# Performance work log

Measured on AMD Instinct MI355X. Metric: run time of the kernel, lower is better.

The kernel has to match this reference:

```python
import jax, jax.numpy as jnp
import numpy as np

MD = 512      # Md = input_dim[0] * ds
L = 31        # spectral bands
SHOTS = 1
HO = jnp.array([0.25, 0.5, 0.25], dtype=jnp.float32)


def spectral_conv3(x, axis):
    # SAME-padded 1x1x3 conv along the spectral axis with symmetric kernel HO.
    # (tf.nn.conv3d and tf.nn.conv3d_transpose coincide for this symmetric kernel.)
    pad = [(0, 0)] * x.ndim
    pad[axis] = (1, 1)
    xp = jnp.pad(x, pad)
    sl = lambda s: tuple(s if a == axis else slice(None) for a in range(x.ndim))
    return HO[0] * xp[sl(slice(0, -2))] + HO[1] * xp[sl(slice(1, -1))] + HO[2] * xp[sl(slice(2, None))]


def setup_inputs() -> dict:
    key = jax.random.key(0)
    k1, k2, k3 = jax.random.split(key, 3)
    X = jax.random.uniform(k1, (1, 1024, 1024, L), dtype=jnp.float32)
    y = jax.random.uniform(k2, (1, MD, MD + L - 1, SHOTS), dtype=jnp.float32)
    H = jax.random.uniform(k3, (1, MD, MD, L, SHOTS), dtype=jnp.float32)
    return {"X": X, "y": y, "H": H}


def reference(X, y, H):
    B = X.shape[0]
    C = MD + L - 1  # detector width after dispersion
    # tf.image.resize (bilinear, half-pixel) -> jax.image.resize bilinear
    Xr = jax.image.resize(X, (B, MD, MD, L), method='bilinear')
    # spectral blur: conv3d with kernel [1,1,3] = HO, SAME padding
    Xc = spectral_conv3(Xr, axis=3)                      # [B,MD,MD,L]
    Xm = H * Xc[..., None]                               # [B,MD,MD,L,S]
    # pad dispersion axis then shear-sum: yn[.,c,s] = sum_i Xm[., c-i, i, s]
    Xp = jnp.pad(Xm, ((0, 0), (0, 0), (0, L - 1), (0, 0), (0, 0)))  # [B,MD,C,L,S]
    cc = jnp.arange(C)
    ii = jnp.arange(L)
    idx = (cc[:, None] - ii[None, :]) % C                # [C,L] roll-with-zero-fill
    yn = Xp[:, :, idx, ii, :].sum(axis=3)                # [B,MD,C,S]
    yn = yn / jnp.max(yn)
    r = yn - y                                           # residual on the detector
    # adjoint shear: Xn[.,c,i,s] = r[., c+i, s]
    idx2 = jnp.arange(MD)[:, None] + ii[None, :]         # [MD,L], max = C-1 (no wrap)
    Xn = r[:, :, idx2, :]                                # [B,MD,MD,L,S]
    # adjoint spectral blur (conv3d_transpose, symmetric kernel == same conv)
    X2 = spectral_conv3(Xn, axis=3)                      # [B,MD,MD,L,S]
    X2 = (H * X2).sum(axis=4)                            # [B,MD,MD,L]
    return X2 / jnp.max(X2)
```

## Files before the change

kernel.cpp:

```cpp
#include <hip/hip_runtime.h>

#define MDIM 512
#define LCH  31
#define CDIM 542
#define INW  1024
#define RS   (INW*LCH)
#define NELEM (MDIM*MDIM*LCH)
#define GB3  2048

#define TNK  32
#define NT   16
#define NPAIR 256

#define PART_OFF 0
#define PART_SZ  (NPAIR*NT*2*128)
#define YN_OFF   (PART_OFF + PART_SZ)
#define PMY_OFF  (YN_OFF + MDIM*CDIM)
#define PMT_OFF  (PMY_OFF + MDIM)
#define SCL_OFF  (PMT_OFF + GB3)

__global__ __launch_bounds__(256) void k1_fused(const float* __restrict__ X,
                                                const float* __restrict__ H,
                                                float* __restrict__ part) {
    __shared__ float xv[2][2048];
    __shared__ float xm[2][32][33];

    const int bid = blockIdx.x;
    const int t   = bid & (NT-1);
    const int p   = bid >> 4;
    const int n0  = t * TNK;
    const int m0  = 2*p;
    const int tid = threadIdx.x;
    const int qa  = 1984*t - 32;

    const float* rp0 = X + (size_t)max(4*p - 1, 0) * RS;
    const float* rp1 = X + (size_t)(4*p    ) * RS;
    const float* rp2 = X + (size_t)(4*p + 1) * RS;
    const float* rp3 = X + (size_t)(4*p + 2) * RS;
    const float* rp4 = X + (size_t)(4*p + 3) * RS;
    const float* rp5 = X + (size_t)min(4*p + 4, INW-1) * RS;

    float wa0=0.125f, wa1=0.375f, wa2=0.375f, wa3=0.125f;
    if (m0 == 0) {
        const float s = 1.0f/0.875f;
        wa0 = 0.f; wa1 = 0.375f*s; wa2 = 0.375f*s; wa3 = 0.125f*s;
    }
    float wb0=0.125f, wb1=0.375f, wb2=0.375f, wb3=0.125f;
    if (m0 + 1 == MDIM-1) {
        const float s = 1.0f/0.875f;
        wb0 = 0.125f*s; wb1 = 0.375f*s; wb2 = 0.375f*s; wb3 = 0.f;
    }

    #pragma unroll
    for (int j = 0; j < 2; ++j) {
        const int u = tid + 256*j;
        int q = qa + 4*u;
        q = min(max(q, 0), RS - 4);
        const float4 r0 = *(const float4*)(rp0 + q);
        const float4 r1 = *(const float4*)(rp1 + q);
        const float4 r2 = *(const float4*)(rp2 + q);
        const float4 r3 = *(const float4*)(rp3 + q);
        const float4 r4 = *(const float4*)(rp4 + q);
        const float4 r5 = *(const float4*)(rp5 + q);
        float4 va, vb;
        va.x = fmaf(wa0,r0.x, fmaf(wa1,r1.x, fmaf(wa2,r2.x, wa3*r3.x)));
        va.y = fmaf(wa0,r0.y, fmaf(wa1,r1.y, fmaf(wa2,r2.y, wa3*r3.y)));
        va.z = fmaf(wa0,r0.z, fmaf(wa1,r1.z, fmaf(wa2,r2.z, wa3*r3.z)));
        va.w = fmaf(wa0,r0.w, fmaf(wa1,r1.w, fmaf(wa2,r2.w, wa3*r3.w)));
        vb.x = fmaf(wb0,r2.x, fmaf(wb1,r3.x, fmaf(wb2,r4.x, wb3*r5.x)));
        vb.y = fmaf(wb0,r2.y, fmaf(wb1,r3.y, fmaf(wb2,r4.y, wb3*r5.y)));
        vb.z = fmaf(wb0,r2.z, fmaf(wb1,r3.z, fmaf(wb2,r4.z, wb3*r5.z)));
        vb.w = fmaf(wb0,r2.w, fmaf(wb1,r3.w, fmaf(wb2,r4.w, wb3*r5.w)));
        *(float4*)&xv[0][4*u] = va;
        *(float4*)&xv[1][4*u] = vb;
    }
    __syncthreads();

    const size_t hbase = ((size_t)m0*MDIM + n0)*LCH;
    for (int idx = tid; idx < 2*TNK*LCH; idx += 256) {
        const int mm = idx >= TNK*LCH;
        const int r2 = mm ? idx - TNK*LCH : idx;
        const int nl = r2 / 31;
        const int l  = r2 - nl*31;
        const int n  = n0 + nl;
        float wx0=0.125f, wx1=0.375f, wx2=0.375f, wx3=0.125f;
        if (n == 0)      wx0 = 0.f;
        if (n == MDIM-1) wx3 = 0.f;
        if (n == 0 || n == MDIM-1) {
            const float s = 1.0f/0.875f;
            wx0*=s; wx1*=s; wx2*=s; wx3*=s;
        }
        const float wb4[4] = {wx0, wx1, wx2, wx3};
        const float* xvm = xv[mm];
        const int ib = 2*nl*31 + l + 1;
        float acc = 0.f;
        #pragma unroll
        for (int b = 0; b < 4; ++b) {
            const float* q = xvm + ib + 31*b;
            float c = 0.5f*q[0];
            if (l > 0)  c += 0.25f*q[-1];
            if (l < 30) c += 0.25f*q[1];
            acc = fmaf(wb4[b], c, acc);
        }
        const float hv = H[hbase + (size_t)mm*(MDIM*LCH) + r2];
        xm[mm][nl][l] = acc * hv;
    }
    __syncthreads();

    if (tid < 248) {
        const int mm = tid >= 124;
        const int r3 = mm ? tid - 124 : tid;
        const int h  = r3 >= 62;
        const int cl = h ? r3 - 62 : r3;
        const int ilo = max(0, cl - (TNK-1));
        const int ihi = min(30, cl);
        const int mid = (ilo + ihi + 1) >> 1;
        const int lo  = h ? mid : ilo;
        const int hi  = h ? ihi : mid - 1;
        float s = 0.f;
        for (int i = lo; i <= hi; ++i)
            s += xm[mm][cl - i][i];
        part[(((size_t)p*NT + t)*2 + mm)*128 + h*64 + cl] = s;
    }
}

__global__ __launch_bounds__(256) void k2_lite(const float* __restrict__ part,
                                               float* __restrict__ yn,
                                               float* __restrict__ pmaxY) {
    const int m = blockIdx.x;
    const int p = m >> 1, mm = m & 1;
    float lmax = -3.4e38f;
    for (int c = threadIdx.x; c < CDIM; c += 256) {
        float s = 0.f;
        const int tlo = max(0, (c - 30) >> 5);
        const int thi = min(NT - 1, c >> 5);
        for (int t = tlo; t <= thi; ++t) {
            const int cl = c - TNK*t;
            const float* pp = part + (((size_t)p*NT + t)*2 + mm)*128;
            s += pp[cl] + pp[64 + cl];
        }
        yn[m*CDIM + c] = s;
        lmax = fmaxf(lmax, s);
    }
    __shared__ float red[256];
    red[threadIdx.x] = lmax; __syncthreads();
    for (int s = 128; s > 0; s >>= 1) {
        if ((int)threadIdx.x < s)
            red[threadIdx.x] = fmaxf(red[threadIdx.x], red[threadIdx.x+s]);
        __syncthreads();
    }
    if (threadIdx.x == 0) pmaxY[m] = red[0];
}

__global__ __launch_bounds__(256) void kmax_reduce(const float* __restrict__ pmax,
                                                   int n,
                                                   float* __restrict__ out_inv) {
    __shared__ float red[256];
    float lmax = -3.4e38f;
    for (int i = threadIdx.x; i < n; i += 256)
        lmax = fmaxf(lmax, pmax[i]);
    red[threadIdx.x] = lmax; __syncthreads();
    for (int s = 128; s > 0; s >>= 1) {
        if ((int)threadIdx.x < s)
            red[threadIdx.x] = fmaxf(red[threadIdx.x], red[threadIdx.x+s]);
        __syncthreads();
    }
    if (threadIdx.x == 0) out_inv[0] = 1.0f / red[0];
}

__device__ __forceinline__ float t_elem(int idx,
                                        const float* __restrict__ yn,
                                        const float* __restrict__ y,
                                        const float* __restrict__ H,
                                        float inv) {
    const int i    = idx % LCH;
    const int rest = idx / LCH;
    const int n    = rest & (MDIM-1);
    const int m    = rest >> 9;
    const int c    = n + i;
    const float* ynr = yn + (size_t)m*CDIM;
    const float* yr  = y  + (size_t)m*CDIM;
    float v = 0.5f * (ynr[c]*inv - yr[c]);
    if (i > 0)     v += 0.25f*(ynr[c-1]*inv - yr[c-1]);
    if (i < LCH-1) v += 0.25f*(ynr[c+1]*inv - yr[c+1]);
    return H[idx]*v;
}

__global__ __launch_bounds__(256) void k3_max(const float* __restrict__ yn,
                                              const float* __restrict__ y,
                                              const float* __restrict__ H,
                                              const float* __restrict__ scl,
                                              float* __restrict__ pmaxT) {
    const float inv = scl[0];
    float lmax = -3.4e38f;
    for (int idx = blockIdx.x*blockDim.x + threadIdx.x; idx < NELEM;
         idx += GB3*256)
        lmax = fmaxf(lmax, t_elem(idx, yn, y, H, inv));
    __shared__ float red[256];
    red[threadIdx.x] = lmax; __syncthreads();
    for (int s = 128; s > 0; s >>= 1) {
        if ((int)threadIdx.x < s)
            red[threadIdx.x] = fmaxf(red[threadIdx.x], red[threadIdx.x+s]);
        __syncthreads();
    }
    if (threadIdx.x == 0) pmaxT[blockIdx.x] = red[0];
}

__global__ __launch_bounds__(256) void k4_out(const float* __restrict__ yn,
                                              const float* __restrict__ y,
                                              const float* __restrict__ H,
                                              const float* __restrict__ scl,
                                              float* __restrict__ out) {
    const float inv  = scl[0];
    const float invT = scl[1];
    for (int idx = blockIdx.x*blockDim.x + threadIdx.x; idx < NELEM;
         idx += GB3*256)
        out[idx] = t_elem(idx, yn, y, H, inv) * invT;
}

extern "C" void kernel_launch(void* const* d_in, const int* in_sizes, int n_in,
                              void* d_out, int out_size, void* d_ws, size_t ws_size,
                              hipStream_t stream) {
    const float* X = (const float*)d_in[0];
    const float* y = (const float*)d_in[1];
    const float* H = (const float*)d_in[2];
    float* out = (float*)d_out;
    float* ws  = (float*)d_ws;

    float* part  = ws + PART_OFF;
    float* yn    = ws + YN_OFF;
    float* pmaxY = ws + PMY_OFF;
    float* pmaxT = ws + PMT_OFF;
    float* scl   = ws + SCL_OFF;

    k1_fused<<<NPAIR*NT, 256, 0, stream>>>(X, H, part);
    k2_lite<<<MDIM, 256, 0, stream>>>(part, yn, pmaxY);
    kmax_reduce<<<1, 256, 0, stream>>>(pmaxY, MDIM, scl);
    k3_max<<<GB3, 256, 0, stream>>>(yn, y, H, scl, pmaxT);
    kmax_reduce<<<1, 256, 0, stream>>>(pmaxT, GB3, scl + 1);
    k4_out<<<GB3, 256, 0, stream>>>(yn, y, H, scl, out);
}
```

Before: 90.79 us.

## Process four output rows per block and fold max reductions into last-block epilogues

```diff
diff --git a/kernel.cpp b/kernel.cpp
--- a/kernel.cpp
+++ b/kernel.cpp
@@ -10,76 +10,76 @@
 
 #define TNK  32
 #define NT   16
-#define NPAIR 256
+#define MGRP 4
+#define NQ   128
 
 #define PART_OFF 0
-#define PART_SZ  (NPAIR*NT*2*128)
+#define PART_SZ  (NQ*NT*MGRP*128)
 #define YN_OFF   (PART_OFF + PART_SZ)
 #define PMY_OFF  (YN_OFF + MDIM*CDIM)
 #define PMT_OFF  (PMY_OFF + MDIM)
 #define SCL_OFF  (PMT_OFF + GB3)
+#define CNT_OFF  (SCL_OFF + 2)
 
 __global__ __launch_bounds__(256) void k1_fused(const float* __restrict__ X,
                                                 const float* __restrict__ H,
-                                                float* __restrict__ part) {
-    __shared__ float xv[2][2048];
-    __shared__ float xm[2][32][33];
+                                                float* __restrict__ part,
+                                                int* __restrict__ cnt) {
+    __shared__ float xv[MGRP][2048];
+    __shared__ float xm[MGRP][32][33];
 
     const int bid = blockIdx.x;
     const int t   = bid & (NT-1);
-    const int p   = bid >> 4;
+    const int g   = bid >> 4;
     const int n0  = t * TNK;
-    const int m0  = 2*p;
     const int tid = threadIdx.x;
     const int qa  = 1984*t - 32;
 
-    const float* rp0 = X + (size_t)max(4*p - 1, 0) * RS;
-    const float* rp1 = X + (size_t)(4*p    ) * RS;
-    const float* rp2 = X + (size_t)(4*p + 1) * RS;
-    const float* rp3 = X + (size_t)(4*p + 2) * RS;
-    const float* rp4 = X + (size_t)(4*p + 3) * RS;
-    const float* rp5 = X + (size_t)min(4*p + 4, INW-1) * RS;
-
-    float wa0=0.125f, wa1=0.375f, wa2=0.375f, wa3=0.125f;
-    if (m0 == 0) {
-        const float s = 1.0f/0.875f;
-        wa0 = 0.f; wa1 = 0.375f*s; wa2 = 0.375f*s; wa3 = 0.125f*s;
-    }
-    float wb0=0.125f, wb1=0.375f, wb2=0.375f, wb3=0.125f;
-    if (m0 + 1 == MDIM-1) {
-        const float s = 1.0f/0.875f;
-        wb0 = 0.125f*s; wb1 = 0.375f*s; wb2 = 0.375f*s; wb3 = 0.f;
-    }
+    if (bid == 0 && tid < 2) cnt[tid] = 0;
+
+    float W[4][4];
+    #pragma unroll
+    for (int k = 0; k < 4; ++k) {
+        W[k][0]=0.125f; W[k][1]=0.375f; W[k][2]=0.375f; W[k][3]=0.125f;
+    }
+    if (g == 0)      { const float s=1.0f/0.875f; W[0][0]=0.f; W[0][1]=0.375f*s; W[0][2]=0.375f*s; W[0][3]=0.125f*s; }
+    if (g == NQ-1)   { const float s=1.0f/0.875f; W[3][3]=0.f; W[3][0]=0.125f*s; W[3][1]=0.375f*s; W[3][2]=0.375f*s; }
+
+    const float* rowp[10];
+    #pragma unroll
+    for (int rr = 0; rr < 10; ++rr)
+        rowp[rr] = X + (size_t)min(max(8*g - 1 + rr, 0), INW-1) * RS;
 
     #pragma unroll
     for (int j = 0; j < 2; ++j) {
         const int u = tid + 256*j;
-        int q = qa + 4*u;
-        q = min(max(q, 0), RS - 4);
-        const float4 r0 = *(const float4*)(rp0 + q);
-        const float4 r1 = *(const float4*)(rp1 + q);
-        const float4 r2 = *(const float4*)(rp2 + q);
-        const float4 r3 = *(const float4*)(rp3 + q);
-        const float4 r4 = *(const float4*)(rp4 + q);
-        const float4 r5 = *(const float4*)(rp5 + q);
-        float4 va, vb;
-        va.x = fmaf(wa0,r0.x, fmaf(wa1,r1.x, fmaf(wa2,r2.x, wa3*r3.x)));
-        va.y = fmaf(wa0,r0.y, fmaf(wa1,r1.y, fmaf(wa2,r2.y, wa3*r3.y)));
-        va.z = fmaf(wa0,r0.z, fmaf(wa1,r1.z, fmaf(wa2,r2.z, wa3*r3.z)));
-        va.w = fmaf(wa0,r0.w, fmaf(wa1,r1.w, fmaf(wa2,r2.w, wa3*r3.w)));
-        vb.x = fmaf(wb0,r2.x, fmaf(wb1,r3.x, fmaf(wb2,r4.x, wb3*r5.x)));
-        vb.y = fmaf(wb0,r2.y, fmaf(wb1,r3.y, fmaf(wb2,r4.y, wb3*r5.y)));
-        vb.z = fmaf(wb0,r2.z, fmaf(wb1,r3.z, fmaf(wb2,r4.z, wb3*r5.z)));
-        vb.w = fmaf(wb0,r2.w, fmaf(wb1,r3.w, fmaf(wb2,r4.w, wb3*r5.w)));
-        *(float4*)&xv[0][4*u] = va;
-        *(float4*)&xv[1][4*u] = vb;
-    }
-    __syncthreads();
-
-    const size_t hbase = ((size_t)m0*MDIM + n0)*LCH;
-    for (int idx = tid; idx < 2*TNK*LCH; idx += 256) {
-        const int mm = idx >= TNK*LCH;
-        const int r2 = mm ? idx - TNK*LCH : idx;
+        const int q = min(max(qa + 4*u, 0), RS - 4);
+        float4 acc[4];
+        #pragma unroll
+        for (int k = 0; k < 4; ++k) acc[k] = make_float4(0.f,0.f,0.f,0.f);
+        #pragma unroll
+        for (int rr = 0; rr < 10; ++rr) {
+            const float4 r = *(const float4*)(rowp[rr] + q);
+            #pragma unroll
+            for (int k = 0; k < 4; ++k) {
+                if (rr >= 2*k && rr <= 2*k + 3) {
+                    const float w = W[k][rr - 2*k];
+                    acc[k].x = fmaf(w, r.x, acc[k].x);
+                    acc[k].y = fmaf(w, r.y, acc[k].y);
+                    acc[k].z = fmaf(w, r.z, acc[k].z);
+                    acc[k].w = fmaf(w, r.w, acc[k].w);
+                }
+            }
+        }
+        #pragma unroll
+        for (int k = 0; k < 4; ++k) *(float4*)&xv[k][4*u] = acc[k];
+    }
+    __syncthreads();
+
+    const size_t hbase = ((size_t)(MGRP*g)*MDIM + n0)*LCH;
+    for (int idx = tid; idx < MGRP*TNK*LCH; idx += 256) {
+        const int mm = idx / (TNK*LCH);
+        const int r2 = idx - mm*(TNK*LCH);
         const int nl = r2 / 31;
         const int l  = r2 - nl*31;
         const int n  = n0 + nl;
@@ -102,33 +102,37 @@
             if (l < 30) c += 0.25f*q[1];
             acc = fmaf(wb4[b], c, acc);
         }
-        const float hv = H[hbase + (size_t)mm*(MDIM*LCH) + r2];
-        xm[mm][nl][l] = acc * hv;
-    }
-    __syncthreads();
-
-    if (tid < 248) {
-        const int mm = tid >= 124;
-        const int r3 = mm ? tid - 124 : tid;
-        const int h  = r3 >= 62;
-        const int cl = h ? r3 - 62 : r3;
-        const int ilo = max(0, cl - (TNK-1));
-        const int ihi = min(30, cl);
-        const int mid = (ilo + ihi + 1) >> 1;
-        const int lo  = h ? mid : ilo;
-        const int hi  = h ? ihi : mid - 1;
-        float s = 0.f;
-        for (int i = lo; i <= hi; ++i)
-            s += xm[mm][cl - i][i];
-        part[(((size_t)p*NT + t)*2 + mm)*128 + h*64 + cl] = s;
+        xm[mm][nl][l] = acc * H[hbase + (size_t)mm*(MDIM*LCH) + r2];
+    }
+    __syncthreads();
+
+    for (int base = 0; base < 496; base += 256) {
+        const int idx = base + tid;
+        if (idx < 496) {
+            const int mm = idx / 124;
+            const int r3 = idx - mm*124;
+            const int h  = r3 >= 62;
+            const int cl = h ? r3 - 62 : r3;
+            const int ilo = max(0, cl - (TNK-1));
+            const int ihi = min(30, cl);
+            const int mid = (ilo + ihi + 1) >> 1;
+            const int lo  = h ? mid : ilo;
+            const int hi  = h ? ihi : mid - 1;
+            float s = 0.f;
+            for (int i = lo; i <= hi; ++i)
+                s += xm[mm][cl - i][i];
+            part[(((size_t)g*NT + t)*MGRP + mm)*128 + h*64 + cl] = s;
+        }
     }
 }
 
 __global__ __launch_bounds__(256) void k2_lite(const float* __restrict__ part,
                                                float* __restrict__ yn,
-                                               float* __restrict__ pmaxY) {
+                                               float* __restrict__ pmaxY,
+                                               float* __restrict__ scl,
+                                               int* __restrict__ cnt) {
     const int m = blockIdx.x;
-    const int p = m >> 1, mm = m & 1;
+    const int g = m >> 2, mm = m & 3;
     float lmax = -3.4e38f;
     for (int c = threadIdx.x; c < CDIM; c += 256) {
         float s = 0.f;
@@ -136,36 +140,39 @@
         const int thi = min(NT - 1, c >> 5);
         for (int t = tlo; t <= thi; ++t) {
             const int cl = c - TNK*t;
-            const float* pp = part + (((size_t)p*NT + t)*2 + mm)*128;
+            const float* pp = part + (((size_t)g*NT + t)*MGRP + mm)*128;
             s += pp[cl] + pp[64 + cl];
         }
         yn[m*CDIM + c] = s;
         lmax = fmaxf(lmax, s);
     }
     __shared__ float red[256];
+    __shared__ int isLast;
     red[threadIdx.x] = lmax; __syncthreads();
     for (int s = 128; s > 0; s >>= 1) {
         if ((int)threadIdx.x < s)
             red[threadIdx.x] = fmaxf(red[threadIdx.x], red[threadIdx.x+s]);
         __syncthreads();
     }
-    if (threadIdx.x == 0) pmaxY[m] = red[0];
-}
-
-__global__ __launch_bounds__(256) void kmax_reduce(const float* __restrict__ pmax,
-                                                   int n,
-                                                   float* __restrict__ out_inv) {
-    __shared__ float red[256];
-    float lmax = -3.4e38f;
-    for (int i = threadIdx.x; i < n; i += 256)
-        lmax = fmaxf(lmax, pmax[i]);
-    red[threadIdx.x] = lmax; __syncthreads();
-    for (int s = 128; s > 0; s >>= 1) {
-        if ((int)threadIdx.x < s)
-            red[threadIdx.x] = fmaxf(red[threadIdx.x], red[threadIdx.x+s]);
-        __syncthreads();
-    }
-    if (threadIdx.x == 0) out_inv[0] = 1.0f / red[0];
+    if (threadIdx.x == 0) {
+        pmaxY[m] = red[0];
+        __threadfence();
+        isLast = (atomicAdd(cnt + 0, 1) == (int)gridDim.x - 1);
+    }
+    __syncthreads();
+    if (isLast) {
+        __threadfence();
+        float lm = -3.4e38f;
+        for (int i = threadIdx.x; i < MDIM; i += 256)
+            lm = fmaxf(lm, pmaxY[i]);
+        red[threadIdx.x] = lm; __syncthreads();
+        for (int s = 128; s > 0; s >>= 1) {
+            if ((int)threadIdx.x < s)
+                red[threadIdx.x] = fmaxf(red[threadIdx.x], red[threadIdx.x+s]);
+            __syncthreads();
+        }
+        if (threadIdx.x == 0) { scl[0] = 1.0f / red[0]; cnt[0] = 0; }
+    }
 }
 
 __device__ __forceinline__ float t_elem(int idx,
@@ -189,21 +196,41 @@
 __global__ __launch_bounds__(256) void k3_max(const float* __restrict__ yn,
                                               const float* __restrict__ y,
                                               const float* __restrict__ H,
-                                              const float* __restrict__ scl,
-                                              float* __restrict__ pmaxT) {
+                                              float* __restrict__ scl,
+                                              float* __restrict__ pmaxT,
+                                              int* __restrict__ cnt) {
     const float inv = scl[0];
     float lmax = -3.4e38f;
     for (int idx = blockIdx.x*blockDim.x + threadIdx.x; idx < NELEM;
          idx += GB3*256)
         lmax = fmaxf(lmax, t_elem(idx, yn, y, H, inv));
     __shared__ float red[256];
+    __shared__ int isLast;
     red[threadIdx.x] = lmax; __syncthreads();
     for (int s = 128; s > 0; s >>= 1) {
         if ((int)threadIdx.x < s)
             red[threadIdx.x] = fmaxf(red[threadIdx.x], red[threadIdx.x+s]);
         __syncthreads();
     }
-    if (threadIdx.x == 0) pmaxT[blockIdx.x] = red[0];
+    if (threadIdx.x == 0) {
+        pmaxT[blockIdx.x] = red[0];
+        __threadfence();
+        isLast = (atomicAdd(cnt + 1, 1) == (int)gridDim.x - 1);
+    }
+    __syncthreads();
+    if (isLast) {
+        __threadfence();
+        float lm = -3.4e38f;
+        for (int i = threadIdx.x; i < GB3; i += 256)
+            lm = fmaxf(lm, pmaxT[i]);
+        red[threadIdx.x] = lm; __syncthreads();
+        for (int s = 128; s > 0; s >>= 1) {
+            if ((int)threadIdx.x < s)
+                red[threadIdx.x] = fmaxf(red[threadIdx.x], red[threadIdx.x+s]);
+            __syncthreads();
+        }
+        if (threadIdx.x == 0) { scl[1] = 1.0f / red[0]; cnt[1] = 0; }
+    }
 }
 
 __global__ __launch_bounds__(256) void k4_out(const float* __restrict__ yn,
@@ -232,11 +259,10 @@
     float* pmaxY = ws + PMY_OFF;
     float* pmaxT = ws + PMT_OFF;
     float* scl   = ws + SCL_OFF;
-
-    k1_fused<<<NPAIR*NT, 256, 0, stream>>>(X, H, part);
-    k2_lite<<<MDIM, 256, 0, stream>>>(part, yn, pmaxY);
-    kmax_reduce<<<1, 256, 0, stream>>>(pmaxY, MDIM, scl);
-    k3_max<<<GB3, 256, 0, stream>>>(yn, y, H, scl, pmaxT);
-    kmax_reduce<<<1, 256, 0, stream>>>(pmaxT, GB3, scl + 1);
+    int*   cnt   = (int*)(ws + CNT_OFF);
+
+    k1_fused<<<NQ*NT, 256, 0, stream>>>(X, H, part, cnt);
+    k2_lite<<<MDIM, 256, 0, stream>>>(part, yn, pmaxY, scl, cnt);
+    k3_max<<<GB3, 256, 0, stream>>>(yn, y, H, scl, pmaxT, cnt);
     k4_out<<<GB3, 256, 0, stream>>>(yn, y, H, scl, out);
 }
```

New measurement: 155.1 us. 70.9% more time.

## Stage X rows via async global-to-LDS loads and fold max reductions into consumers

Applied to the files above, without the earlier changes.

```diff
diff --git a/kernel.cpp b/kernel.cpp
--- a/kernel.cpp
+++ b/kernel.cpp
@@ -11,34 +11,56 @@
 #define TNK  32
 #define NT   16
 #define NPAIR 256
+#define SEG  2048
 
 #define PART_OFF 0
 #define PART_SZ  (NPAIR*NT*2*128)
 #define YN_OFF   (PART_OFF + PART_SZ)
 #define PMY_OFF  (YN_OFF + MDIM*CDIM)
 #define PMT_OFF  (PMY_OFF + MDIM)
-#define SCL_OFF  (PMT_OFF + GB3)
+
+typedef const __attribute__((address_space(1))) void* gas_ptr;
+typedef __attribute__((address_space(3))) void* las_ptr;
+__device__ __forceinline__ void gload16(const float* g, float* l) {
+    __builtin_amdgcn_global_load_lds((gas_ptr)g, (las_ptr)l, 16, 0, 0);
+}
 
 __global__ __launch_bounds__(256) void k1_fused(const float* __restrict__ X,
                                                 const float* __restrict__ H,
                                                 float* __restrict__ part) {
-    __shared__ float xv[2][2048];
+    __shared__ float rows[6][SEG];
+    __shared__ float xv[2][SEG];
     __shared__ float xm[2][32][33];
 
-    const int bid = blockIdx.x;
-    const int t   = bid & (NT-1);
-    const int p   = bid >> 4;
-    const int n0  = t * TNK;
-    const int m0  = 2*p;
-    const int tid = threadIdx.x;
-    const int qa  = 1984*t - 32;
-
-    const float* rp0 = X + (size_t)max(4*p - 1, 0) * RS;
-    const float* rp1 = X + (size_t)(4*p    ) * RS;
-    const float* rp2 = X + (size_t)(4*p + 1) * RS;
-    const float* rp3 = X + (size_t)(4*p + 2) * RS;
-    const float* rp4 = X + (size_t)(4*p + 3) * RS;
-    const float* rp5 = X + (size_t)min(4*p + 4, INW-1) * RS;
+    const int bid  = blockIdx.x;
+    const int t    = bid & (NT-1);
+    const int p    = bid >> 4;
+    const int n0   = t * TNK;
+    const int m0   = 2*p;
+    const int tid  = threadIdx.x;
+    const int wave = tid >> 6;
+    const int lane = tid & 63;
+    const int qa   = 1984*t - 32;
+
+    for (int i = wave; i < 48; i += 4) {
+        const int r = i >> 3, c = i & 7;
+        const int u = (c << 6) + lane;
+        const int q = min(max(qa + 4*u, 0), RS - 4);
+        const float* src = X + (size_t)min(max(4*p - 1 + r, 0), INW-1)*RS + q;
+        gload16(src, &rows[r][c << 8]);
+    }
+
+    const size_t hbase = ((size_t)m0*MDIM + n0)*LCH;
+    float harr[8];
+    #pragma unroll
+    for (int k = 0; k < 8; ++k) {
+        int idx = tid + (k << 8);
+        if (idx >= 2*TNK*LCH) idx = 2*TNK*LCH - 1;
+        const int mm = idx >= TNK*LCH;
+        const int r2 = mm ? idx - TNK*LCH : idx;
+        harr[k] = H[hbase + (size_t)mm*(MDIM*LCH) + r2];
+    }
+    __syncthreads();
 
     float wa0=0.125f, wa1=0.375f, wa2=0.375f, wa3=0.125f;
     if (m0 == 0) {
@@ -50,60 +72,56 @@
         const float s = 1.0f/0.875f;
         wb0 = 0.125f*s; wb1 = 0.375f*s; wb2 = 0.375f*s; wb3 = 0.f;
     }
-
     #pragma unroll
-    for (int j = 0; j < 2; ++j) {
-        const int u = tid + 256*j;
-        int q = qa + 4*u;
-        q = min(max(q, 0), RS - 4);
-        const float4 r0 = *(const float4*)(rp0 + q);
-        const float4 r1 = *(const float4*)(rp1 + q);
-        const float4 r2 = *(const float4*)(rp2 + q);
-        const float4 r3 = *(const float4*)(rp3 + q);
-        const float4 r4 = *(const float4*)(rp4 + q);
-        const float4 r5 = *(const float4*)(rp5 + q);
-        float4 va, vb;
-        va.x = fmaf(wa0,r0.x, fmaf(wa1,r1.x, fmaf(wa2,r2.x, wa3*r3.x)));
-        va.y = fmaf(wa0,r0.y, fmaf(wa1,r1.y, fmaf(wa2,r2.y, wa3*r3.y)));
-        va.z = fmaf(wa0,r0.z, fmaf(wa1,r1.z, fmaf(wa2,r2.z, wa3*r3.z)));
-        va.w = fmaf(wa0,r0.w, fmaf(wa1,r1.w, fmaf(wa2,r2.w, wa3*r3.w)));
-        vb.x = fmaf(wb0,r2.x, fmaf(wb1,r3.x, fmaf(wb2,r4.x, wb3*r5.x)));
-        vb.y = fmaf(wb0,r2.y, fmaf(wb1,r3.y, fmaf(wb2,r4.y, wb3*r5.y)));
-        vb.z = fmaf(wb0,r2.z, fmaf(wb1,r3.z, fmaf(wb2,r4.z, wb3*r5.z)));
-        vb.w = fmaf(wb0,r2.w, fmaf(wb1,r3.w, fmaf(wb2,r4.w, wb3*r5.w)));
-        *(float4*)&xv[0][4*u] = va;
-        *(float4*)&xv[1][4*u] = vb;
-    }
-    __syncthreads();
-
-    const size_t hbase = ((size_t)m0*MDIM + n0)*LCH;
-    for (int idx = tid; idx < 2*TNK*LCH; idx += 256) {
-        const int mm = idx >= TNK*LCH;
-        const int r2 = mm ? idx - TNK*LCH : idx;
-        const int nl = r2 / 31;
-        const int l  = r2 - nl*31;
-        const int n  = n0 + nl;
-        float wx0=0.125f, wx1=0.375f, wx2=0.375f, wx3=0.125f;
-        if (n == 0)      wx0 = 0.f;
-        if (n == MDIM-1) wx3 = 0.f;
-        if (n == 0 || n == MDIM-1) {
-            const float s = 1.0f/0.875f;
-            wx0*=s; wx1*=s; wx2*=s; wx3*=s;
+    for (int j = 0; j < 4; ++j) {
+        const int u4 = tid + (j << 8);
+        const int mm = u4 >> 9;
+        const int uu = u4 & 511;
+        const float4 r0 = *(const float4*)&rows[2*mm + 0][4*uu];
+        const float4 r1 = *(const float4*)&rows[2*mm + 1][4*uu];
+        const float4 r2 = *(const float4*)&rows[2*mm + 2][4*uu];
+        const float4 r3 = *(const float4*)&rows[2*mm + 3][4*uu];
+        const float w0 = mm ? wb0 : wa0, w1 = mm ? wb1 : wa1;
+        const float w2 = mm ? wb2 : wa2, w3 = mm ? wb3 : wa3;
+        float4 v;
+        v.x = fmaf(w0,r0.x, fmaf(w1,r1.x, fmaf(w2,r2.x, w3*r3.x)));
+        v.y = fmaf(w0,r0.y, fmaf(w1,r1.y, fmaf(w2,r2.y, w3*r3.y)));
+        v.z = fmaf(w0,r0.z, fmaf(w1,r1.z, fmaf(w2,r2.z, w3*r3.z)));
+        v.w = fmaf(w0,r0.w, fmaf(w1,r1.w, fmaf(w2,r2.w, w3*r3.w)));
+        *(float4*)&xv[mm][4*uu] = v;
+    }
+    __syncthreads();
+
+    #pragma unroll
+    for (int k = 0; k < 8; ++k) {
+        const int idx = tid + (k << 8);
+        if (idx < 2*TNK*LCH) {
+            const int mm = idx >= TNK*LCH;
+            const int r2 = mm ? idx - TNK*LCH : idx;
+            const int nl = r2 / 31;
+            const int l  = r2 - nl*31;
+            const int n  = n0 + nl;
+            float wx0=0.125f, wx1=0.375f, wx2=0.375f, wx3=0.125f;
+            if (n == 0)      wx0 = 0.f;
+            if (n == MDIM-1) wx3 = 0.f;
+            if (n == 0 || n == MDIM-1) {
+                const float s = 1.0f/0.875f;
+                wx0*=s; wx1*=s; wx2*=s; wx3*=s;
+            }
+            const float wb4[4] = {wx0, wx1, wx2, wx3};
+            const float* xvm = xv[mm];
+            const int ib = 2*nl*31 + l + 1;
+            float acc = 0.f;
+            #pragma unroll
+            for (int b = 0; b < 4; ++b) {
+                const float* q = xvm + ib + 31*b;
+                float c = 0.5f*q[0];
+                if (l > 0)  c += 0.25f*q[-1];
+                if (l < 30) c += 0.25f*q[1];
+                acc = fmaf(wb4[b], c, acc);
+            }
+            xm[mm][nl][l] = acc * harr[k];
         }
-        const float wb4[4] = {wx0, wx1, wx2, wx3};
-        const float* xvm = xv[mm];
-        const int ib = 2*nl*31 + l + 1;
-        float acc = 0.f;
-        #pragma unroll
-        for (int b = 0; b < 4; ++b) {
-            const float* q = xvm + ib + 31*b;
-            float c = 0.5f*q[0];
-            if (l > 0)  c += 0.25f*q[-1];
-            if (l < 30) c += 0.25f*q[1];
-            acc = fmaf(wb4[b], c, acc);
-        }
-        const float hv = H[hbase + (size_t)mm*(MDIM*LCH) + r2];
-        xm[mm][nl][l] = acc * hv;
     }
     __syncthreads();
 
@@ -152,20 +170,19 @@
     if (threadIdx.x == 0) pmaxY[m] = red[0];
 }
 
-__global__ __launch_bounds__(256) void kmax_reduce(const float* __restrict__ pmax,
-                                                   int n,
-                                                   float* __restrict__ out_inv) {
-    __shared__ float red[256];
-    float lmax = -3.4e38f;
+__device__ __forceinline__ float block_max_of(const float* __restrict__ arr,
+                                              int n, float* red) {
+    float lm = -3.4e38f;
     for (int i = threadIdx.x; i < n; i += 256)
-        lmax = fmaxf(lmax, pmax[i]);
-    red[threadIdx.x] = lmax; __syncthreads();
+        lm = fmaxf(lm, arr[i]);
+    __syncthreads();
+    red[threadIdx.x] = lm; __syncthreads();
     for (int s = 128; s > 0; s >>= 1) {
         if ((int)threadIdx.x < s)
             red[threadIdx.x] = fmaxf(red[threadIdx.x], red[threadIdx.x+s]);
         __syncthreads();
     }
-    if (threadIdx.x == 0) out_inv[0] = 1.0f / red[0];
+    return red[0];
 }
 
 __device__ __forceinline__ float t_elem(int idx,
@@ -189,14 +206,15 @@
 __global__ __launch_bounds__(256) void k3_max(const float* __restrict__ yn,
                                               const float* __restrict__ y,
                                               const float* __restrict__ H,
-                                              const float* __restrict__ scl,
+                                              const float* __restrict__ pmaxY,
                                               float* __restrict__ pmaxT) {
-    const float inv = scl[0];
+    __shared__ float red[256];
+    const float invY = 1.0f / block_max_of(pmaxY, MDIM, red);
     float lmax = -3.4e38f;
     for (int idx = blockIdx.x*blockDim.x + threadIdx.x; idx < NELEM;
          idx += GB3*256)
-        lmax = fmaxf(lmax, t_elem(idx, yn, y, H, inv));
-    __shared__ float red[256];
+        lmax = fmaxf(lmax, t_elem(idx, yn, y, H, invY));
+    __syncthreads();
     red[threadIdx.x] = lmax; __syncthreads();
     for (int s = 128; s > 0; s >>= 1) {
         if ((int)threadIdx.x < s)
@@ -209,13 +227,16 @@
 __global__ __launch_bounds__(256) void k4_out(const float* __restrict__ yn,
                                               const float* __restrict__ y,
                                               const float* __restrict__ H,
-                                              const float* __restrict__ scl,
+                                              const float* __restrict__ pmaxY,
+                                              const float* __restrict__ pmaxT,
                                               float* __restrict__ out) {
-    const float inv  = scl[0];
-    const float invT = scl[1];
+    __shared__ float red[256];
+    const float invY = 1.0f / block_max_of(pmaxY, MDIM, red);
+    __syncthreads();
+    const float invT = 1.0f / block_max_of(pmaxT, GB3, red);
     for (int idx = blockIdx.x*blockDim.x + threadIdx.x; idx < NELEM;
          idx += GB3*256)
-        out[idx] = t_elem(idx, yn, y, H, inv) * invT;
+        out[idx] = t_elem(idx, yn, y, H, invY) * invT;
 }
 
 extern "C" void kernel_launch(void* const* d_in, const int* in_sizes, int n_in,
@@ -231,12 +252,9 @@
     float* yn    = ws + YN_OFF;
     float* pmaxY = ws + PMY_OFF;
     float* pmaxT = ws + PMT_OFF;
-    float* scl   = ws + SCL_OFF;
 
     k1_fused<<<NPAIR*NT, 256, 0, stream>>>(X, H, part);
     k2_lite<<<MDIM, 256, 0, stream>>>(part, yn, pmaxY);
-    kmax_reduce<<<1, 256, 0, stream>>>(pmaxY, MDIM, scl);
-    k3_max<<<GB3, 256, 0, stream>>>(yn, y, H, scl, pmaxT);
-    kmax_reduce<<<1, 256, 0, stream>>>(pmaxT, GB3, scl + 1);
-    k4_out<<<GB3, 256, 0, stream>>>(yn, y, H, scl, out);
-}
+    k3_max<<<GB3, 256, 0, stream>>>(yn, y, H, pmaxY, pmaxT);
+    k4_out<<<GB3, 256, 0, stream>>>(yn, y, H, pmaxY, pmaxT, out);
+}
```

New measurement: 113.7 us. +25.3%, slower.

## Fold max reductions into consumer kernels and vectorize elementwise passes with float4

Applied to the files above, without the earlier changes.

```diff
diff --git a/kernel.cpp b/kernel.cpp
--- a/kernel.cpp
+++ b/kernel.cpp
@@ -6,6 +6,7 @@
 #define INW  1024
 #define RS   (INW*LCH)
 #define NELEM (MDIM*MDIM*LCH)
+#define NV4  (NELEM/4)
 #define GB3  2048
 
 #define TNK  32
@@ -17,7 +18,6 @@
 #define YN_OFF   (PART_OFF + PART_SZ)
 #define PMY_OFF  (YN_OFF + MDIM*CDIM)
 #define PMT_OFF  (PMY_OFF + MDIM)
-#define SCL_OFF  (PMT_OFF + GB3)
 
 __global__ __launch_bounds__(256) void k1_fused(const float* __restrict__ X,
                                                 const float* __restrict__ H,
@@ -102,8 +102,7 @@
             if (l < 30) c += 0.25f*q[1];
             acc = fmaf(wb4[b], c, acc);
         }
-        const float hv = H[hbase + (size_t)mm*(MDIM*LCH) + r2];
-        xm[mm][nl][l] = acc * hv;
+        xm[mm][nl][l] = acc * H[hbase + (size_t)mm*(MDIM*LCH) + r2];
     }
     __syncthreads();
 
@@ -152,70 +151,91 @@
     if (threadIdx.x == 0) pmaxY[m] = red[0];
 }
 
-__global__ __launch_bounds__(256) void kmax_reduce(const float* __restrict__ pmax,
-                                                   int n,
-                                                   float* __restrict__ out_inv) {
+__device__ __forceinline__ float block_max_of(const float* __restrict__ arr,
+                                              int n, float* red) {
+    float lm = -3.4e38f;
+    for (int i = threadIdx.x; i < n; i += 256)
+        lm = fmaxf(lm, arr[i]);
+    __syncthreads();
+    red[threadIdx.x] = lm; __syncthreads();
+    for (int s = 128; s > 0; s >>= 1) {
+        if ((int)threadIdx.x < s)
+            red[threadIdx.x] = fmaxf(red[threadIdx.x], red[threadIdx.x+s]);
+        __syncthreads();
+    }
+    return red[0];
+}
+
+template <bool STORE>
+__device__ __forceinline__ float t_quad(int v4,
+                                        const float* __restrict__ yn,
+                                        const float* __restrict__ y,
+                                        const float* __restrict__ H,
+                                        float invY, float invT,
+                                        float* __restrict__ out) {
+    const int idx = v4 << 2;
+    const float4 h = *(const float4*)(H + idx);
+    const float hv[4] = {h.x, h.y, h.z, h.w};
+    int i    = idx % LCH;
+    int rest = idx / LCH;
+    int n    = rest & (MDIM-1);
+    int m    = rest >> 9;
+    float tv[4];
+    float lmax = -3.4e38f;
+    #pragma unroll
+    for (int e = 0; e < 4; ++e) {
+        const float* ynr = yn + m*CDIM;
+        const float* yr  = y  + m*CDIM;
+        const int c = n + i;
+        float v = 0.5f * (ynr[c]*invY - yr[c]);
+        if (i > 0)       v += 0.25f*(ynr[c-1]*invY - yr[c-1]);
+        if (i < LCH-1)   v += 0.25f*(ynr[c+1]*invY - yr[c+1]);
+        tv[e] = hv[e]*v;
+        lmax = fmaxf(lmax, tv[e]);
+        if (++i == LCH) { i = 0; if (++n == MDIM) { n = 0; ++m; } }
+    }
+    if (STORE) {
+        float4 o; o.x = tv[0]*invT; o.y = tv[1]*invT;
+        o.z = tv[2]*invT; o.w = tv[3]*invT;
+        *(float4*)(out + idx) = o;
+    }
+    return lmax;
+}
+
+__global__ __launch_bounds__(256) void k3_max(const float* __restrict__ yn,
+                                              const float* __restrict__ y,
+                                              const float* __restrict__ H,
+                                              const float* __restrict__ pmaxY,
+                                              float* __restrict__ pmaxT) {
     __shared__ float red[256];
+    const float invY = 1.0f / block_max_of(pmaxY, MDIM, red);
     float lmax = -3.4e38f;
-    for (int i = threadIdx.x; i < n; i += 256)
-        lmax = fmaxf(lmax, pmax[i]);
+    for (int v4 = blockIdx.x*blockDim.x + threadIdx.x; v4 < NV4;
+         v4 += GB3*256)
+        lmax = fmaxf(lmax, t_quad<false>(v4, yn, y, H, invY, 0.f, nullptr));
+    __syncthreads();
     red[threadIdx.x] = lmax; __syncthreads();
     for (int s = 128; s > 0; s >>= 1) {
         if ((int)threadIdx.x < s)
             red[threadIdx.x] = fmaxf(red[threadIdx.x], red[threadIdx.x+s]);
         __syncthreads();
     }
-    if (threadIdx.x == 0) out_inv[0] = 1.0f / red[0];
-}
-
-__device__ __forceinline__ float t_elem(int idx,
-                                        const float* __restrict__ yn,
-                                        const float* __restrict__ y,
-                                        const float* __restrict__ H,
-                                        float inv) {
-    const int i    = idx % LCH;
-    const int rest = idx / LCH;
-    const int n    = rest & (MDIM-1);
-    const int m    = rest >> 9;
-    const int c    = n + i;
-    const float* ynr = yn + (size_t)m*CDIM;
-    const float* yr  = y  + (size_t)m*CDIM;
-    float v = 0.5f * (ynr[c]*inv - yr[c]);
-    if (i > 0)     v += 0.25f*(ynr[c-1]*inv - yr[c-1]);
-    if (i < LCH-1) v += 0.25f*(ynr[c+1]*inv - yr[c+1]);
-    return H[idx]*v;
-}
-
-__global__ __launch_bounds__(256) void k3_max(const float* __restrict__ yn,
-                                              const float* __restrict__ y,
-                                              const float* __restrict__ H,
-                                              const float* __restrict__ scl,
-                                              float* __restrict__ pmaxT) {
-    const float inv = scl[0];
-    float lmax = -3.4e38f;
-    for (int idx = blockIdx.x*blockDim.x + threadIdx.x; idx < NELEM;
-         idx += GB3*256)
-        lmax = fmaxf(lmax, t_elem(idx, yn, y, H, inv));
-    __shared__ float red[256];
-    red[threadIdx.x] = lmax; __syncthreads();
-    for (int s = 128; s > 0; s >>= 1) {
-        if ((int)threadIdx.x < s)
-            red[threadIdx.x] = fmaxf(red[threadIdx.x], red[threadIdx.x+s]);
-        __syncthreads();
-    }
     if (threadIdx.x == 0) pmaxT[blockIdx.x] = red[0];
 }
 
 __global__ __launch_bounds__(256) void k4_out(const float* __restrict__ yn,
                                               const float* __restrict__ y,
                                               const float* __restrict__ H,
-                                              const float* __restrict__ scl,
+                                              const float* __restrict__ pmaxY,
+                                              const float* __restrict__ pmaxT,
                                               float* __restrict__ out) {
-    const float inv  = scl[0];
-    const float invT = scl[1];
-    for (int idx = blockIdx.x*blockDim.x + threadIdx.x; idx < NELEM;
-         idx += GB3*256)
-        out[idx] = t_elem(idx, yn, y, H, inv) * invT;
+    __shared__ float red[256];
+    const float invY = 1.0f / block_max_of(pmaxY, MDIM, red);
+    __syncthreads();
+    const float invT = 1.0f / block_max_of(pmaxT, GB3, red);
+    for (int v4 = blockIdx.x*blockDim.x + threadIdx.x; v4 < NV4;
+         v4 += GB3*256)
+        t_quad<true>(v4, yn, y, H, invY, invT, out);
 }
 
 extern "C" void kernel_launch(void* const* d_in, const int* in_sizes, int n_in,
@@ -231,12 +251,9 @@
     float* yn    = ws + YN_OFF;
     float* pmaxY = ws + PMY_OFF;
     float* pmaxT = ws + PMT_OFF;
-    float* scl   = ws + SCL_OFF;
 
     k1_fused<<<NPAIR*NT, 256, 0, stream>>>(X, H, part);
     k2_lite<<<MDIM, 256, 0, stream>>>(part, yn, pmaxY);
-    kmax_reduce<<<1, 256, 0, stream>>>(pmaxY, MDIM, scl);
-    k3_max<<<GB3, 256, 0, stream>>>(yn, y, H, scl, pmaxT);
-    kmax_reduce<<<1, 256, 0, stream>>>(pmaxT, GB3, scl + 1);
-    k4_out<<<GB3, 256, 0, stream>>>(yn, y, H, scl, out);
-}
+    k3_max<<<GB3, 256, 0, stream>>>(yn, y, H, pmaxY, pmaxT);
+    k4_out<<<GB3, 256, 0, stream>>>(yn, y, H, pmaxY, pmaxT, out);
+}
```

After: 100.1 us. 10.2% more time.
